# Kernel tuning notes

Hardware: AMD Instinct MI355X
Metric: run time of the kernel (lower is better)

The kernel has to match this reference:

```python
import jax, jax.numpy as jnp
import numpy as np

VOCAB, N_EMBD, BLOCK = 50257, 384, 2048
B, T = 4, 2048


def setup_inputs() -> dict:
    key = jax.random.key(0)
    ks = jax.random.split(key, 9)
    s = 0.02
    return {
        "idx": jax.random.randint(ks[0], (B, T), 0, VOCAB),
        "targets": jax.random.randint(ks[1], (B, T), 0, VOCAB),
        "tok_emb": jax.random.normal(ks[2], (VOCAB, N_EMBD), jnp.float32) * s,
        "pos_emb": jax.random.normal(ks[3], (BLOCK, N_EMBD), jnp.float32) * s,
        "Wk": jax.random.normal(ks[4], (N_EMBD, N_EMBD), jnp.float32) * s,  # stored (in,out)
        "Wq": jax.random.normal(ks[5], (N_EMBD, N_EMBD), jnp.float32) * s,
        "Wv": jax.random.normal(ks[6], (N_EMBD, N_EMBD), jnp.float32) * s,
        "W_head": jax.random.normal(ks[7], (N_EMBD, VOCAB), jnp.float32) * s,
        "b_head": jnp.zeros((VOCAB,), jnp.float32),
    }


def reference(idx, targets, tok_emb, pos_emb, Wk, Wq, Wv, W_head, b_head):
    Bb, Tt = idx.shape
    C = tok_emb.shape[1]
    x = tok_emb[idx] + pos_emb[:Tt]                      # [B,T,C]
    K = x @ Wk
    Q = x @ Wq
    V = x @ Wv
    scores = jnp.einsum('btc,bsc->bts', Q, K) / jnp.sqrt(jnp.float32(C))
    causal = jnp.tril(jnp.ones((Tt, Tt), dtype=bool))
    scores = jnp.where(causal, scores, -jnp.inf)
    weights = jax.nn.softmax(scores, axis=-1)
    out = jnp.einsum('bts,bsc->btc', weights, V)          # [B,T,C]
    logits = out @ W_head + b_head                        # [B,T,V]
    logits2d = logits.reshape(Bb * Tt, -1)
    tgt = targets.reshape(-1)
    logp = jax.nn.log_softmax(logits2d, axis=-1)
    loss = -jnp.mean(jnp.take_along_axis(logp, tgt[:, None], axis=1))
    return (logits2d, loss)
```

## Files before the change

kernel.cpp:

```cpp
#include <hip/hip_runtime.h>
#include <hip/hip_bf16.h>

#define AS1 __attribute__((address_space(1)))
#define AS3 __attribute__((address_space(3)))

typedef __bf16 bf16x8 __attribute__((ext_vector_type(8)));
typedef float  f32x4  __attribute__((ext_vector_type(4)));

__device__ __forceinline__ unsigned short f2b(float f) {
    union { __hip_bfloat16 h; unsigned short u; } v;
    v.h = __float2bfloat16(f);
    return v.u;
}

__device__ __forceinline__ void gload16(const void* g, void* l) {
    __builtin_amdgcn_global_load_lds((AS1 void*)(unsigned long long)g,
                                     (AS3 void*)(unsigned int)(unsigned long long)l,
                                     16, 0, 0);
}

__device__ __forceinline__ void block_sync() {
    __builtin_amdgcn_sched_barrier(0);
    asm volatile("" ::: "memory");
    __builtin_amdgcn_s_barrier();
    asm volatile("" ::: "memory");
    __builtin_amdgcn_sched_barrier(0);
}

__device__ __forceinline__ void gemm128_core(
    const char* Asrc, int ldaB,
    const char* Bsrc, int ldbB,
    int ksteps,
    unsigned short* lA, unsigned short* lB,
    f32x4 acc[4][4])
{
    const int tid  = threadIdx.x;
    const int wave = tid >> 6;
    const int lane = tid & 63;
    const int wm = wave >> 1, wn = wave & 1;

    const int c0 = 2 * wave, c1 = 2 * wave + 1;
    const int srowl = lane & 15;
    const int skb   = (lane >> 4) * 16;

    const char* a00 = Asrc + (size_t)(c0 * 16 + srowl) * ldaB + skb;
    const char* a10 = Asrc + (size_t)(c1 * 16 + srowl) * ldaB + skb;
    const char* b00 = Bsrc + (size_t)(c0 * 16 + srowl) * ldbB + skb;
    const char* b10 = Bsrc + (size_t)(c1 * 16 + srowl) * ldbB + skb;

#define STAGE(BOFF) do { \
        gload16(a00,      lA + (BOFF) + c0 * 1024); \
        gload16(a00 + 64, lA + (BOFF) + c0 * 1024 + 512); \
        gload16(a10,      lA + (BOFF) + c1 * 1024); \
        gload16(a10 + 64, lA + (BOFF) + c1 * 1024 + 512); \
        gload16(b00,      lB + (BOFF) + c0 * 1024); \
        gload16(b00 + 64, lB + (BOFF) + c0 * 1024 + 512); \
        gload16(b10,      lB + (BOFF) + c1 * 1024); \
        gload16(b10 + 64, lB + (BOFF) + c1 * 1024 + 512); \
        a00 += 128; a10 += 128; b00 += 128; b10 += 128; } while (0)

    STAGE(0);

    for (int ks = 0; ks < ksteps; ++ks) {
        const int cur = ks & 1;
        if (ks + 1 < ksteps) {
            STAGE((cur ^ 1) * 8192);
            asm volatile("s_waitcnt vmcnt(8)" ::: "memory");
        } else {
            asm volatile("s_waitcnt vmcnt(0)" ::: "memory");
        }
        __builtin_amdgcn_sched_barrier(0);
        __builtin_amdgcn_s_barrier();
        __builtin_amdgcn_sched_barrier(0);
        asm volatile("" ::: "memory");

        const unsigned short* rA = lA + cur * 8192;
        const unsigned short* rB = lB + cur * 8192;
        bf16x8 af[4][2], bg[4][2];
#pragma unroll
        for (int m = 0; m < 4; ++m)
#pragma unroll
            for (int kh = 0; kh < 2; ++kh)
                af[m][kh] = *(const bf16x8*)(rA + (wm * 4 + m) * 1024 + kh * 512 + lane * 8);
#pragma unroll
        for (int n = 0; n < 4; ++n)
#pragma unroll
            for (int kh = 0; kh < 2; ++kh)
                bg[n][kh] = *(const bf16x8*)(rB + (wn * 4 + n) * 1024 + kh * 512 + lane * 8);

        __builtin_amdgcn_s_setprio(1);
#pragma unroll
        for (int kh = 0; kh < 2; ++kh)
#pragma unroll
            for (int m = 0; m < 4; ++m)
#pragma unroll
                for (int n = 0; n < 4; ++n)
                    acc[m][n] = __builtin_amdgcn_mfma_f32_16x16x32_bf16(af[m][kh], bg[n][kh], acc[m][n], 0, 0, 0);
        __builtin_amdgcn_s_setprio(0);

        __builtin_amdgcn_sched_barrier(0);
        asm volatile("" ::: "memory");
        __builtin_amdgcn_s_barrier();
        __builtin_amdgcn_sched_barrier(0);
    }
#undef STAGE
}

__global__ __launch_bounds__(384) void k_embed(
    const int* __restrict__ idx, const float* __restrict__ tok,
    const float* __restrict__ pos, unsigned short* __restrict__ xb)
{
    const int i = blockIdx.x;
    const int c = threadIdx.x;
    const int t = i & 2047;
    float v = tok[(size_t)idx[i] * 384 + c] + pos[(size_t)t * 384 + c];
    xb[(size_t)i * 384 + c] = f2b(v);
}

__global__ __launch_bounds__(256) void k_wt_all(
    const float* __restrict__ Wq, const float* __restrict__ Wk,
    const float* __restrict__ Wv, unsigned short* __restrict__ wt)
{
    int gid = blockIdx.x * 256 + threadIdx.x;
    if (gid >= 1152 * 384) return;
    int n = gid / 384, k = gid % 384;
    const float* W; int col;
    if (n < 384)      { W = Wq; col = n; }
    else if (n < 768) { W = Wk; col = n - 384; }
    else              { W = Wv; col = n - 768; }
    wt[gid] = f2b(W[(size_t)k * 384 + col]);
}

__global__ __launch_bounds__(256) void k_wht(
    const float* __restrict__ Wh, unsigned short* __restrict__ wht)
{
    __shared__ unsigned short tile[32][33];
    const int n0 = blockIdx.x * 32, k0 = blockIdx.y * 32;
    const int tx = threadIdx.x, ty = threadIdx.y;
#pragma unroll
    for (int yy = ty; yy < 32; yy += 8) {
        int n = n0 + tx;
        float v = (n < 50257) ? Wh[(size_t)(k0 + yy) * 50257 + n] : 0.f;
        tile[yy][tx] = f2b(v);
    }
    __syncthreads();
#pragma unroll
    for (int yy = ty; yy < 32; yy += 8)
        wht[(size_t)(n0 + yy) * 384 + k0 + tx] = tile[tx][yy];
}

__global__ __launch_bounds__(256) void k_vt(
    const unsigned short* __restrict__ qkv, unsigned short* __restrict__ vt)
{
    __shared__ unsigned short tile[32][33];
    const int t0 = blockIdx.x * 32, c0 = blockIdx.y * 32, b = blockIdx.z;
    const int tx = threadIdx.x, ty = threadIdx.y;
#pragma unroll
    for (int yy = ty; yy < 32; yy += 8)
        tile[yy][tx] = qkv[((size_t)b * 2048 + t0 + yy) * 1152 + 768 + c0 + tx];
    __syncthreads();
#pragma unroll
    for (int yy = ty; yy < 32; yy += 8)
        vt[((size_t)b * 384 + c0 + yy) * 2048 + t0 + tx] = tile[tx][yy];
}

__global__ __launch_bounds__(256) void k_gemm_qkv(
    const unsigned short* __restrict__ xb, const unsigned short* __restrict__ wt,
    unsigned short* __restrict__ qkv)
{
    __shared__ unsigned short lA[16384], lB[16384];
    const int brow = blockIdx.x * 128;
    const int bcol = blockIdx.y * 128;
    f32x4 acc[4][4] = {};
    gemm128_core((const char*)(xb + (size_t)brow * 384), 768,
                 (const char*)(wt + (size_t)bcol * 384), 768, 6, lA, lB, acc);
    const int tid = threadIdx.x, wave = tid >> 6, lane = tid & 63;
    const int wm = wave >> 1, wn = wave & 1, l15 = lane & 15, l4 = lane >> 4;
#pragma unroll
    for (int m = 0; m < 4; ++m)
#pragma unroll
        for (int n = 0; n < 4; ++n)
#pragma unroll
            for (int r = 0; r < 4; ++r) {
                int row = brow + wm * 64 + m * 16 + l4 * 4 + r;
                int col = bcol + wn * 64 + n * 16 + l15;
                qkv[(size_t)row * 1152 + col] = f2b(acc[m][n][r]);
            }
}

__global__ __launch_bounds__(256) void k_gemm_scores(
    const unsigned short* __restrict__ qkv, float* __restrict__ scores)
{
    const int j = blockIdx.x, i = blockIdx.y, b = blockIdx.z;
    if (j > i) return;
    __shared__ unsigned short lA[16384], lB[16384];
    f32x4 acc[4][4] = {};
    const unsigned short* Q = qkv + ((size_t)b * 2048 + i * 128) * 1152;
    const unsigned short* K = qkv + ((size_t)b * 2048 + j * 128) * 1152 + 384;
    gemm128_core((const char*)Q, 2304, (const char*)K, 2304, 6, lA, lB, acc);
    const int tid = threadIdx.x, wave = tid >> 6, lane = tid & 63;
    const int wm = wave >> 1, wn = wave & 1, l15 = lane & 15, l4 = lane >> 4;
    const float sc = 0.0510310363f;
#pragma unroll
    for (int m = 0; m < 4; ++m)
#pragma unroll
        for (int n = 0; n < 4; ++n)
#pragma unroll
            for (int r = 0; r < 4; ++r) {
                int t = i * 128 + wm * 64 + m * 16 + l4 * 4 + r;
                int s = j * 128 + wn * 64 + n * 16 + l15;
                float v = (s <= t) ? acc[m][n][r] * sc : -1e30f;
                scores[((size_t)b * 2048 + t) * 2048 + s] = v;
            }
}

__global__ __launch_bounds__(256) void k_softmax(float* __restrict__ scores)
{
    const int row = blockIdx.x;
    const int t = row & 2047;
    const int Send = ((t >> 7) + 1) << 7;
    const int tid = threadIdx.x, lane = tid & 63, wave = tid >> 6;
    float* srow = scores + (size_t)row * 2048;
    unsigned short* wrow = (unsigned short*)scores + (size_t)row * 4096;

    float vals[8]; int cnt = 0;
    float sum = 0.f;
    for (int s = tid; s < Send; s += 256) {
        float e = __expf(srow[s]);
        vals[cnt++] = e; sum += e;
    }
    __shared__ float red[4];
#pragma unroll
    for (int off = 32; off; off >>= 1) sum += __shfl_xor(sum, off);
    if (lane == 0) red[wave] = sum;
    __syncthreads();
    sum = red[0] + red[1] + red[2] + red[3];

    float inv = 1.f / sum;
    int k2 = 0;
    for (int s = tid; s < Send; s += 256) wrow[s] = f2b(vals[k2++] * inv);
}

__global__ __launch_bounds__(256) void k_gemm_pv(
    const float* __restrict__ scores, const unsigned short* __restrict__ vt,
    unsigned short* __restrict__ outb)
{
    const int x = blockIdx.x;
    const int i = blockIdx.y;
    const int b = blockIdx.z;
    __shared__ unsigned short lA[16384], lB[16384];
    f32x4 acc[4][4] = {};
    const unsigned short* A = (const unsigned short*)scores + ((size_t)b * 2048 + i * 128) * 4096;
    const unsigned short* B = vt + ((size_t)b * 384 + x * 128) * 2048;
    gemm128_core((const char*)A, 8192, (const char*)B, 4096, (i + 1) * 2, lA, lB, acc);
    const int tid = threadIdx.x, wave = tid >> 6, lane = tid & 63;
    const int wm = wave >> 1, wn = wave & 1, l15 = lane & 15, l4 = lane >> 4;
#pragma unroll
    for (int m = 0; m < 4; ++m)
#pragma unroll
        for (int n = 0; n < 4; ++n)
#pragma unroll
            for (int r = 0; r < 4; ++r) {
                int row = b * 2048 + i * 128 + wm * 64 + m * 16 + l4 * 4 + r;
                int col = x * 128 + wn * 64 + n * 16 + l15;
                outb[(size_t)row * 384 + col] = f2b(acc[m][n][r]);
            }
}

__global__ __launch_bounds__(512, 2) void k_gemm_head(
    const unsigned short* __restrict__ outb, const unsigned short* __restrict__ wht,
    const float* __restrict__ bhead, float* __restrict__ logits,
    float* __restrict__ ps)
{
    const int i  = blockIdx.x;
    const int jn = blockIdx.y;
    const int brow = i * 256, bcol = jn * 256;
    __shared__ unsigned short lA[32768], lB[32768];

    const int tid  = threadIdx.x;
    const int wave = tid >> 6;
    const int lane = tid & 63;
    const int wm = wave >> 2;
    const int wn = wave & 3;

    const int c0 = 2 * wave, c1 = 2 * wave + 1;
    const int srowl = lane & 15;
    const int skb   = (lane >> 4) * 16;

    const char* Asrc = (const char*)(outb + (size_t)brow * 384);
    const char* Bsrc = (const char*)(wht + (size_t)bcol * 384);

    const char* a0 = Asrc + (size_t)(c0 * 16 + srowl) * 768 + skb;
    const char* a1 = Asrc + (size_t)(c1 * 16 + srowl) * 768 + skb;
    const char* b0 = Bsrc + (size_t)(c0 * 16 + srowl) * 768 + skb;
    const char* b1 = Bsrc + (size_t)(c1 * 16 + srowl) * 768 + skb;

    f32x4 acc[8][4] = {};

    {
        char* dA = (char*)lA; char* dB = (char*)lB;
        gload16(b0,      dB + c0 * 2048);
        gload16(b1,      dB + c1 * 2048);
        gload16(a0,      dA + c0 * 2048);
        gload16(a1,      dA + c1 * 2048);
        gload16(a0 + 64, dA + c0 * 2048 + 1024);
        gload16(a1 + 64, dA + c1 * 2048 + 1024);
        gload16(b0 + 64, dB + c0 * 2048 + 1024);
        gload16(b1 + 64, dB + c1 * 2048 + 1024);
        a0 += 128; a1 += 128; b0 += 128; b1 += 128;
    }
    asm volatile("s_waitcnt vmcnt(4)" ::: "memory");
    block_sync();

#define LDA4(mh, kh) do { \
        const char* _p = rA + ((wm * 8 + (mh) * 4) * 2048 + (kh) * 1024) + lane * 16; \
        af[0] = *(const bf16x8*)(_p); \
        af[1] = *(const bf16x8*)(_p + 2048); \
        af[2] = *(const bf16x8*)(_p + 4096); \
        af[3] = *(const bf16x8*)(_p + 6144); } while (0)
#define LDB4(kh) do { \
        const char* _p = rB + ((wn * 4) * 2048 + (kh) * 1024) + lane * 16; \
        bg[0] = *(const bf16x8*)(_p); \
        bg[1] = *(const bf16x8*)(_p + 2048); \
        bg[2] = *(const bf16x8*)(_p + 4096); \
        bg[3] = *(const bf16x8*)(_p + 6144); } while (0)
#define MFMA16(mh) do { \
        __builtin_amdgcn_s_setprio(1); \
        _Pragma("unroll") \
        for (int _m = 0; _m < 4; ++_m) \
            _Pragma("unroll") \
            for (int _n = 0; _n < 4; ++_n) \
                acc[(mh) * 4 + _m][_n] = __builtin_amdgcn_mfma_f32_16x16x32_bf16( \
                    af[_m], bg[_n], acc[(mh) * 4 + _m][_n], 0, 0, 0); \
        __builtin_amdgcn_s_setprio(0); } while (0)

#pragma unroll 1
    for (int t = 0; t < 5; ++t) {
        const int cur = t & 1;
        const char* rA = (const char*)lA + cur * 32768;
        const char* rB = (const char*)lB + cur * 32768;
        char* sA = (char*)lA + (cur ^ 1) * 32768;
        char* sB = (char*)lB + (cur ^ 1) * 32768;
        bf16x8 af[4], bg[4];

        LDB4(0); LDA4(0, 0);
        gload16(b0, sB + c0 * 2048); gload16(b1, sB + c1 * 2048);
        block_sync();
        MFMA16(0);
        block_sync();

        LDA4(1, 0);
        gload16(a0, sA + c0 * 2048); gload16(a1, sA + c1 * 2048);
        asm volatile("s_waitcnt vmcnt(4)" ::: "memory");
        block_sync();
        MFMA16(1);
        block_sync();

        LDB4(1); LDA4(0, 1);
        gload16(a0 + 64, sA + c0 * 2048 + 1024); gload16(a1 + 64, sA + c1 * 2048 + 1024);
        block_sync();
        MFMA16(0);
        block_sync();

        LDA4(1, 1);
        gload16(b0 + 64, sB + c0 * 2048 + 1024); gload16(b1 + 64, sB + c1 * 2048 + 1024);
        asm volatile("s_waitcnt vmcnt(4)" ::: "memory");
        block_sync();
        MFMA16(1);
        block_sync();

        a0 += 128; a1 += 128; b0 += 128; b1 += 128;
    }
    {
        const char* rA = (const char*)lA + 32768;
        const char* rB = (const char*)lB + 32768;
        bf16x8 af[4], bg[4];

        LDB4(0); LDA4(0, 0);
        block_sync();
        MFMA16(0);
        block_sync();

        LDA4(1, 0);
        asm volatile("s_waitcnt vmcnt(0)" ::: "memory");
        block_sync();
        MFMA16(1);
        block_sync();

        LDB4(1); LDA4(0, 1);
        block_sync();
        MFMA16(0);
        block_sync();

        LDA4(1, 1);
        block_sync();
        MFMA16(1);
        block_sync();
    }
#undef LDA4
#undef LDB4
#undef MFMA16

    const int l15 = lane & 15, l4 = lane >> 4;
    float bv[4]; int cv[4]; bool ok[4];
#pragma unroll
    for (int n = 0; n < 4; ++n) {
        int c = bcol + wn * 64 + n * 16 + l15;
        cv[n] = c;
        ok[n] = (c < 50257);
        bv[n] = ok[n] ? bhead[c] : 0.f;
    }

    float (*part)[64] = (float(*)[64])lA;
#pragma unroll
    for (int m = 0; m < 8; ++m) {
#pragma unroll
        for (int r = 0; r < 4; ++r) {
            int pr = wm * 128 + m * 16 + l4 * 4 + r;
            size_t grow = (size_t)(brow + pr);
            float s = 0.f;
#pragma unroll
            for (int n = 0; n < 4; ++n) {
                float x = acc[m][n][r] + bv[n];
                if (ok[n]) {
                    logits[grow * 50257 + cv[n]] = x;
                    s += __expf(x);
                }
            }
            part[pr][((wn * 16 + l15) + pr) & 63] = s;
        }
    }
    __syncthreads();
    if (tid < 256) {
        float S = 0.f;
#pragma unroll 8
        for (int j = 0; j < 64; ++j) S += part[tid][(j + tid) & 63];
        ps[(size_t)(brow + tid) * 197 + jn] = S;
    }
}

__global__ __launch_bounds__(256) void k_loss_row(
    const float* __restrict__ ps, const float* __restrict__ logits,
    const int* __restrict__ targets, float* __restrict__ rowloss)
{
    const int tid = threadIdx.x;
    const int row = blockIdx.x * 4 + (tid >> 6);
    const int lane = tid & 63;
    float s = 0.f;
    for (int nb = lane; nb < 197; nb += 64) s += ps[(size_t)row * 197 + nb];
#pragma unroll
    for (int off = 32; off; off >>= 1) s += __shfl_xor(s, off);
    if (lane == 0) {
        float lse = logf(s);
        int tg = targets[row];
        float lt = logits[(size_t)row * 50257 + tg];
        rowloss[row] = lse - lt;
    }
}

__global__ __launch_bounds__(256) void k_loss_final(
    const float* __restrict__ rowloss, float* __restrict__ out_loss)
{
    const int tid = threadIdx.x;
    float s = 0.f;
    for (int r = tid; r < 8192; r += 256) s += rowloss[r];
    __shared__ float red2[256];
    red2[tid] = s;
    __syncthreads();
    for (int off = 128; off; off >>= 1) {
        if (tid < off) red2[tid] += red2[tid + off];
        __syncthreads();
    }
    if (tid == 0) out_loss[0] = red2[0] * (1.0f / 8192.0f);
}

extern "C" void kernel_launch(void* const* d_in, const int* in_sizes, int n_in,
                              void* d_out, int out_size, void* d_ws, size_t ws_size,
                              hipStream_t stream)
{
    (void)in_sizes; (void)n_in; (void)out_size; (void)ws_size;
    const int*   idx = (const int*)d_in[0];
    const int*   tgt = (const int*)d_in[1];
    const float* tok = (const float*)d_in[2];
    const float* pos = (const float*)d_in[3];
    const float* Wk  = (const float*)d_in[4];
    const float* Wq  = (const float*)d_in[5];
    const float* Wv  = (const float*)d_in[6];
    const float* Wh  = (const float*)d_in[7];
    const float* bh  = (const float*)d_in[8];

    float* logits = (float*)d_out;
    float* loss   = logits + (size_t)8192 * 50257;

    char* ws = (char*)d_ws;
    unsigned short* xb   = (unsigned short*)(ws + 0);
    unsigned short* wt   = (unsigned short*)(ws + 6291456);
    unsigned short* qkv  = (unsigned short*)(ws + 7176192);
    unsigned short* vt   = (unsigned short*)(ws + 26050560);
    unsigned short* outb = (unsigned short*)(ws + 32342016);
    unsigned short* wht  = (unsigned short*)(ws + 38633472);
    float* scores        = (float*)(ws + 77365248);
    float* psb           = (float*)(ws + 144474112);
    float* rl            = (float*)(ws + 150929408);

    k_embed      <<<dim3(8192),       dim3(384),   0, stream>>>(idx, tok, pos, xb);
    k_wt_all     <<<dim3(1728),       dim3(256),   0, stream>>>(Wq, Wk, Wv, wt);
    k_wht        <<<dim3(1576, 12),   dim3(32, 8), 0, stream>>>(Wh, wht);
    k_gemm_qkv   <<<dim3(64, 9),      dim3(256),   0, stream>>>(xb, wt, qkv);
    k_vt         <<<dim3(64, 12, 4),  dim3(32, 8), 0, stream>>>(qkv, vt);
    k_gemm_scores<<<dim3(16, 16, 4),  dim3(256),   0, stream>>>(qkv, scores);
    k_softmax    <<<dim3(8192),       dim3(256),   0, stream>>>(scores);
    k_gemm_pv    <<<dim3(3, 16, 4),   dim3(256),   0, stream>>>(scores, vt, outb);
    k_gemm_head  <<<dim3(32, 197),    dim3(512),   0, stream>>>(outb, wht, bh, logits, psb);
    k_loss_row   <<<dim3(2048),       dim3(256),   0, stream>>>(psb, logits, tgt, rl);
    k_loss_final <<<dim3(1),          dim3(256),   0, stream>>>(rl, loss);
}
```

Measured before the change: 1.046 ms.

## Pre-tile head GEMM operands into LDS-native blocked layout for contiguous loads

The head-weight transpose and the PV epilogue now write their bf16 outputs directly in the blocked tile layout the head GEMM stages into LDS. The head GEMM then issues contiguous 16-byte loads from a single advancing pointer instead of strided row loads. This aims to make each wave's global_load_lds fetch fully contiguous and cut address arithmetic. In exchange, the transpose kernel reads strided columns with 64 registers per thread, and the PV kernel writes scattered 2-byte stores.

```diff
diff --git a/kernel.cpp b/kernel.cpp
--- a/kernel.cpp
+++ b/kernel.cpp
@@ -6,6 +6,7 @@
 
 typedef __bf16 bf16x8 __attribute__((ext_vector_type(8)));
 typedef float  f32x4  __attribute__((ext_vector_type(4)));
+typedef unsigned short u16x8 __attribute__((ext_vector_type(8)));
 
 __device__ __forceinline__ unsigned short f2b(float f) {
     union { __hip_bfloat16 h; unsigned short u; } v;
@@ -26,6 +27,7 @@
     asm volatile("" ::: "memory");
     __builtin_amdgcn_sched_barrier(0);
 }
+
 
 __device__ __forceinline__ void gemm128_core(
     const char* Asrc, int ldaB,
@@ -132,21 +134,28 @@
 }
 
 __global__ __launch_bounds__(256) void k_wht(
-    const float* __restrict__ Wh, unsigned short* __restrict__ wht)
-{
-    __shared__ unsigned short tile[32][33];
-    const int n0 = blockIdx.x * 32, k0 = blockIdx.y * 32;
-    const int tx = threadIdx.x, ty = threadIdx.y;
-#pragma unroll
-    for (int yy = ty; yy < 32; yy += 8) {
-        int n = n0 + tx;
-        float v = (n < 50257) ? Wh[(size_t)(k0 + yy) * 50257 + n] : 0.f;
-        tile[yy][tx] = f2b(v);
-    }
-    __syncthreads();
-#pragma unroll
-    for (int yy = ty; yy < 32; yy += 8)
-        wht[(size_t)(n0 + yy) * 384 + k0 + tx] = tile[tx][yy];
+    const float* __restrict__ Wh, unsigned short* __restrict__ btile)
+{
+    const int jn = blockIdx.x;
+    const int ks = blockIdx.y;
+    const int r  = threadIdx.x;
+    const int n  = jn * 256 + r;
+    const bool ok = (n < 50257);
+
+    float v[64];
+#pragma unroll
+    for (int kk = 0; kk < 64; ++kk)
+        v[kk] = ok ? Wh[(size_t)(ks * 64 + kk) * 50257 + n] : 0.f;
+
+    const int c = r >> 4, rl = r & 15;
+    unsigned short* base = btile + ((size_t)jn * 6 + ks) * 16384 + c * 1024 + rl * 8;
+#pragma unroll
+    for (int kb = 0; kb < 8; ++kb) {
+        u16x8 pk;
+#pragma unroll
+        for (int e = 0; e < 8; ++e) pk[e] = f2b(v[kb * 8 + e]);
+        *(u16x8*)(base + (kb >> 2) * 512 + (kb & 3) * 128) = pk;
+    }
 }
 
 __global__ __launch_bounds__(256) void k_vt(
@@ -243,7 +252,7 @@
 
 __global__ __launch_bounds__(256) void k_gemm_pv(
     const float* __restrict__ scores, const unsigned short* __restrict__ vt,
-    unsigned short* __restrict__ outb)
+    unsigned short* __restrict__ atile)
 {
     const int x = blockIdx.x;
     const int i = blockIdx.y;
@@ -255,20 +264,29 @@
     gemm128_core((const char*)A, 8192, (const char*)B, 4096, (i + 1) * 2, lA, lB, acc);
     const int tid = threadIdx.x, wave = tid >> 6, lane = tid & 63;
     const int wm = wave >> 1, wn = wave & 1, l15 = lane & 15, l4 = lane >> 4;
-#pragma unroll
-    for (int m = 0; m < 4; ++m)
-#pragma unroll
-        for (int n = 0; n < 4; ++n)
+
+    const int ih = b * 8 + (i >> 1);
+    const int ks = (x * 128 + wn * 64) >> 6;
+    const int e  = l15 & 7;
+#pragma unroll
+    for (int m = 0; m < 4; ++m) {
+        const int c = (i & 1) * 8 + wm * 4 + m;
+#pragma unroll
+        for (int n = 0; n < 4; ++n) {
+            const int w64 = n * 16 + l15;
+            const int kh = w64 >> 5, slot = (w64 & 31) >> 3;
 #pragma unroll
             for (int r = 0; r < 4; ++r) {
-                int row = b * 2048 + i * 128 + wm * 64 + m * 16 + l4 * 4 + r;
-                int col = x * 128 + wn * 64 + n * 16 + l15;
-                outb[(size_t)row * 384 + col] = f2b(acc[m][n][r]);
+                const int rl = l4 * 4 + r;
+                atile[((size_t)(ih * 6 + ks) * 16 + c) * 1024
+                      + kh * 512 + slot * 128 + rl * 8 + e] = f2b(acc[m][n][r]);
             }
+        }
+    }
 }
 
 __global__ __launch_bounds__(512, 2) void k_gemm_head(
-    const unsigned short* __restrict__ outb, const unsigned short* __restrict__ wht,
+    const unsigned short* __restrict__ atile, const unsigned short* __restrict__ btile,
     const float* __restrict__ bhead, float* __restrict__ logits,
     float* __restrict__ ps)
 {
@@ -284,30 +302,23 @@
     const int wn = wave & 3;
 
     const int c0 = 2 * wave, c1 = 2 * wave + 1;
-    const int srowl = lane & 15;
-    const int skb   = (lane >> 4) * 16;
-
-    const char* Asrc = (const char*)(outb + (size_t)brow * 384);
-    const char* Bsrc = (const char*)(wht + (size_t)bcol * 384);
-
-    const char* a0 = Asrc + (size_t)(c0 * 16 + srowl) * 768 + skb;
-    const char* a1 = Asrc + (size_t)(c1 * 16 + srowl) * 768 + skb;
-    const char* b0 = Bsrc + (size_t)(c0 * 16 + srowl) * 768 + skb;
-    const char* b1 = Bsrc + (size_t)(c1 * 16 + srowl) * 768 + skb;
+
+    const char* pa = (const char*)atile + (size_t)i  * 196608 + lane * 16;
+    const char* pb = (const char*)btile + (size_t)jn * 196608 + lane * 16;
 
     f32x4 acc[8][4] = {};
 
     {
         char* dA = (char*)lA; char* dB = (char*)lB;
-        gload16(b0,      dB + c0 * 2048);
-        gload16(b1,      dB + c1 * 2048);
-        gload16(a0,      dA + c0 * 2048);
-        gload16(a1,      dA + c1 * 2048);
-        gload16(a0 + 64, dA + c0 * 2048 + 1024);
-        gload16(a1 + 64, dA + c1 * 2048 + 1024);
-        gload16(b0 + 64, dB + c0 * 2048 + 1024);
-        gload16(b1 + 64, dB + c1 * 2048 + 1024);
-        a0 += 128; a1 += 128; b0 += 128; b1 += 128;
+        gload16(pb + c0 * 2048,        dB + c0 * 2048);
+        gload16(pb + c1 * 2048,        dB + c1 * 2048);
+        gload16(pa + c0 * 2048,        dA + c0 * 2048);
+        gload16(pa + c1 * 2048,        dA + c1 * 2048);
+        gload16(pa + c0 * 2048 + 1024, dA + c0 * 2048 + 1024);
+        gload16(pa + c1 * 2048 + 1024, dA + c1 * 2048 + 1024);
+        gload16(pb + c0 * 2048 + 1024, dB + c0 * 2048 + 1024);
+        gload16(pb + c1 * 2048 + 1024, dB + c1 * 2048 + 1024);
+        pa += 32768; pb += 32768;
     }
     asm volatile("s_waitcnt vmcnt(4)" ::: "memory");
     block_sync();
@@ -344,32 +355,36 @@
         bf16x8 af[4], bg[4];
 
         LDB4(0); LDA4(0, 0);
-        gload16(b0, sB + c0 * 2048); gload16(b1, sB + c1 * 2048);
+        gload16(pb + c0 * 2048, sB + c0 * 2048);
+        gload16(pb + c1 * 2048, sB + c1 * 2048);
         block_sync();
         MFMA16(0);
         block_sync();
 
         LDA4(1, 0);
-        gload16(a0, sA + c0 * 2048); gload16(a1, sA + c1 * 2048);
+        gload16(pa + c0 * 2048, sA + c0 * 2048);
+        gload16(pa + c1 * 2048, sA + c1 * 2048);
         asm volatile("s_waitcnt vmcnt(4)" ::: "memory");
         block_sync();
         MFMA16(1);
         block_sync();
 
         LDB4(1); LDA4(0, 1);
-        gload16(a0 + 64, sA + c0 * 2048 + 1024); gload16(a1 + 64, sA + c1 * 2048 + 1024);
+        gload16(pa + c0 * 2048 + 1024, sA + c0 * 2048 + 1024);
+        gload16(pa + c1 * 2048 + 1024, sA + c1 * 2048 + 1024);
         block_sync();
         MFMA16(0);
         block_sync();
 
         LDA4(1, 1);
-        gload16(b0 + 64, sB + c0 * 2048 + 1024); gload16(b1 + 64, sB + c1 * 2048 + 1024);
+        gload16(pb + c0 * 2048 + 1024, sB + c0 * 2048 + 1024);
+        gload16(pb + c1 * 2048 + 1024, sB + c1 * 2048 + 1024);
         asm volatile("s_waitcnt vmcnt(4)" ::: "memory");
         block_sync();
         MFMA16(1);
         block_sync();
 
-        a0 += 128; a1 += 128; b0 += 128; b1 += 128;
+        pa += 32768; pb += 32768;
     }
     {
         const char* rA = (const char*)lA + 32768;
@@ -493,25 +508,25 @@
     float* loss   = logits + (size_t)8192 * 50257;
 
     char* ws = (char*)d_ws;
-    unsigned short* xb   = (unsigned short*)(ws + 0);
-    unsigned short* wt   = (unsigned short*)(ws + 6291456);
-    unsigned short* qkv  = (unsigned short*)(ws + 7176192);
-    unsigned short* vt   = (unsigned short*)(ws + 26050560);
-    unsigned short* outb = (unsigned short*)(ws + 32342016);
-    unsigned short* wht  = (unsigned short*)(ws + 38633472);
-    float* scores        = (float*)(ws + 77365248);
-    float* psb           = (float*)(ws + 144474112);
-    float* rl            = (float*)(ws + 150929408);
+    unsigned short* xb    = (unsigned short*)(ws + 0);
+    unsigned short* wt    = (unsigned short*)(ws + 6291456);
+    unsigned short* qkv   = (unsigned short*)(ws + 7176192);
+    unsigned short* vt    = (unsigned short*)(ws + 26050560);
+    unsigned short* atile = (unsigned short*)(ws + 32342016);
+    unsigned short* btile = (unsigned short*)(ws + 38633472);
+    float* scores         = (float*)(ws + 77365248);
+    float* psb            = (float*)(ws + 144474112);
+    float* rl             = (float*)(ws + 150929408);
 
     k_embed      <<<dim3(8192),       dim3(384),   0, stream>>>(idx, tok, pos, xb);
     k_wt_all     <<<dim3(1728),       dim3(256),   0, stream>>>(Wq, Wk, Wv, wt);
-    k_wht        <<<dim3(1576, 12),   dim3(32, 8), 0, stream>>>(Wh, wht);
+    k_wht        <<<dim3(197, 6),     dim3(256),   0, stream>>>(Wh, btile);
     k_gemm_qkv   <<<dim3(64, 9),      dim3(256),   0, stream>>>(xb, wt, qkv);
     k_vt         <<<dim3(64, 12, 4),  dim3(32, 8), 0, stream>>>(qkv, vt);
     k_gemm_scores<<<dim3(16, 16, 4),  dim3(256),   0, stream>>>(qkv, scores);
     k_softmax    <<<dim3(8192),       dim3(256),   0, stream>>>(scores);
-    k_gemm_pv    <<<dim3(3, 16, 4),   dim3(256),   0, stream>>>(scores, vt, outb);
-    k_gemm_head  <<<dim3(32, 197),    dim3(512),   0, stream>>>(outb, wht, bh, logits, psb);
+    k_gemm_pv    <<<dim3(3, 16, 4),   dim3(256),   0, stream>>>(scores, vt, atile);
+    k_gemm_head  <<<dim3(32, 197),    dim3(512),   0, stream>>>(atile, btile, bh, logits, psb);
     k_loss_row   <<<dim3(2048),       dim3(256),   0, stream>>>(psb, logits, tgt, rl);
     k_loss_final <<<dim3(1),          dim3(256),   0, stream>>>(rl, loss);
 }
```

Measured after the change: 950.0 us. -9.2%, faster.
